# Optimization experiments

Hardware: AMD Instinct MI355X
Metric: run time of the kernel (lower is better)

Reference implementation:

```python
import jax, jax.numpy as jnp
import numpy as np

B, S, H = 16, 512, 2048
NH, NKV = 16, 4
HD = H // NH  # 128


def _rope_tables(seq_len, dim, dtype):
    inv_freq = 1.0 / (10000.0 ** (jnp.arange(0, dim, 2, dtype=jnp.float32) / dim))
    t = jnp.arange(seq_len, dtype=jnp.float32)
    freqs = jnp.einsum('i,j->ij', t, inv_freq)          # [S, HD/2]
    emb = jnp.concatenate([freqs, freqs], axis=-1)       # [S, HD]
    cos = jnp.cos(emb)[None, None].astype(dtype)         # [1,1,S,HD]
    sin = jnp.sin(emb)[None, None].astype(dtype)
    return cos, sin


def _rotate_half(x):
    x1, x2 = jnp.split(x, 2, axis=-1)
    return jnp.concatenate([-x2, x1], axis=-1)


def setup_inputs() -> dict:
    key = jax.random.key(0)
    kx, kq, kk, kv, ko = jax.random.split(key, 5)
    x = jax.random.normal(kx, (B, S, H), dtype=jnp.float32)
    s = 0.02
    Wq = jax.random.normal(kq, (H, H), dtype=jnp.float32) * s
    Wk = jax.random.normal(kk, (NKV * HD, H), dtype=jnp.float32) * s
    Wv = jax.random.normal(kv, (NKV * HD, H), dtype=jnp.float32) * s
    Wo = jax.random.normal(ko, (H, H), dtype=jnp.float32) * s
    return {"x": x, "Wq": Wq, "Wk": Wk, "Wv": Wv, "Wo": Wo}


def reference(x, Wq, Wk, Wv, Wo):
    b, s, _ = x.shape
    scaling = HD ** -0.5
    # projections (torch Linear: y = x @ W.T, W is [out,in])
    q = jnp.einsum('bsh,oh->bso', x, Wq).reshape(b, s, NH, HD).transpose(0, 2, 1, 3)
    k = jnp.einsum('bsh,oh->bso', x, Wk).reshape(b, s, NKV, HD).transpose(0, 2, 1, 3)
    v = jnp.einsum('bsh,oh->bso', x, Wv).reshape(b, s, NKV, HD).transpose(0, 2, 1, 3)
    cos, sin = _rope_tables(s, HD, x.dtype)
    q = q * cos + _rotate_half(q) * sin
    k = k * cos + _rotate_half(k) * sin
    rep = NH // NKV
    k = jnp.repeat(k, rep, axis=1)  # [b, NH, s, HD]
    v = jnp.repeat(v, rep, axis=1)
    scores = jnp.einsum('bhqd,bhkd->bhqk', q, k) * scaling
    attn = jax.nn.softmax(scores, axis=-1)
    out = jnp.einsum('bhqk,bhkd->bhqd', attn, v)
    out = out.transpose(0, 2, 1, 3).reshape(b, s, H)
    return jnp.einsum('bsh,oh->bso', out, Wo)
```

## Files before the change

### kernel.cpp

```cpp
#include <hip/hip_runtime.h>
#include <stdint.h>


typedef _Float16 f16;
typedef _Float16 f16x4 __attribute__((ext_vector_type(4)));
typedef _Float16 f16x8 __attribute__((ext_vector_type(8)));
typedef float f32x4 __attribute__((ext_vector_type(4)));

#define B_   16
#define S_   512
#define H_   2048
#define NH_  16
#define NKV_ 4
#define HD_  128
#define ATT_SCALE 0.08838834764831843f
#define LOG2_10000_DIV64 0.20762050593045952f

#define AS1 __attribute__((address_space(1)))
#define AS3 __attribute__((address_space(3)))

__device__ __forceinline__ void async16(const void* g, const void* l) {
  __builtin_amdgcn_global_load_lds((const AS1 unsigned int*)(uintptr_t)g,
                                   (AS3 unsigned int*)(uintptr_t)l, 16, 0, 0);
}

__global__ __launch_bounds__(256) void cast_all(const float* __restrict__ x,
                                                const float* __restrict__ wq,
                                                const float* __restrict__ wk,
                                                const float* __restrict__ wv,
                                                const float* __restrict__ wo,
                                                f16* __restrict__ x_h,
                                                f16* __restrict__ w_h,
                                                f16* __restrict__ wo_h) {
  const int i = blockIdx.x * 256 + threadIdx.x;
  const float4* src;
  f16x4* dst;
  if (i < 4194304) {
    src = (const float4*)x + i;            dst = (f16x4*)x_h + i;
  } else if (i < 5242880) {
    int j = i - 4194304;
    src = (const float4*)wq + j;           dst = (f16x4*)w_h + j;
  } else if (i < 5505024) {
    int j = i - 5242880;
    src = (const float4*)wk + j;           dst = (f16x4*)w_h + 1048576 + j;
  } else if (i < 5767168) {
    int j = i - 5505024;
    src = (const float4*)wv + j;           dst = (f16x4*)w_h + 1310720 + j;
  } else {
    int j = i - 5767168;
    src = (const float4*)wo + j;           dst = (f16x4*)wo_h + j;
  }
  float4 v = *src;
  f16x4 o = {(f16)v.x, (f16)v.y, (f16)v.z, (f16)v.w};
  *dst = o;
}

__device__ __forceinline__ int swz(int r, int c) { return c ^ ((r >> 1) & 3); }

__global__ __launch_bounds__(256) void gemm_qkv(const f16* __restrict__ A,
                                                const f16* __restrict__ W,
                                                f16* __restrict__ qo,
                                                f16* __restrict__ ko,
                                                f16* __restrict__ vto) {
  __shared__ __align__(16) f16 As[128 * 32];
  __shared__ __align__(16) f16 Bs[128 * 32];
  const int K = 2048;
  const int m0 = blockIdx.x * 128;
  const int n0 = blockIdx.y * 128;
  const int tid = threadIdx.x;
  const int wave = tid >> 6, lane = tid & 63;
  const int quad = lane >> 4, l15 = lane & 15;
  const int wm = wave >> 1, wn = wave & 1;
  const int G0 = wave * 128 + lane;
  const int r0 = G0 >> 2, c0g = swz(r0, G0 & 3);
  const int r1 = (G0 + 64) >> 2, c1g = swz(r1, (G0 + 64) & 3);

  f32x4 acc[4][4] = {};

  for (int k0 = 0; k0 < K; k0 += 32) {
    async16(A + (size_t)(m0 + r0) * K + k0 + c0g * 8, (const char*)As + (size_t)G0 * 16);
    async16(A + (size_t)(m0 + r1) * K + k0 + c1g * 8, (const char*)As + (size_t)(G0 + 64) * 16);
    async16(W + (size_t)(n0 + r0) * K + k0 + c0g * 8, (const char*)Bs + (size_t)G0 * 16);
    async16(W + (size_t)(n0 + r1) * K + k0 + c1g * 8, (const char*)Bs + (size_t)(G0 + 64) * 16);
    __syncthreads();
    f16x8 a[4], b[4];
#pragma unroll
    for (int mi = 0; mi < 4; ++mi) {
      const int row = wm * 64 + mi * 16 + l15;
      a[mi] = *reinterpret_cast<const f16x8*>(As + row * 32 + swz(row, quad) * 8);
    }
#pragma unroll
    for (int ni = 0; ni < 4; ++ni) {
      const int col = (ni >> 1) * 64 + wn * 32 + (ni & 1) * 16 + l15;
      b[ni] = *reinterpret_cast<const f16x8*>(Bs + col * 32 + swz(col, quad) * 8);
    }
#pragma unroll
    for (int mi = 0; mi < 4; ++mi)
#pragma unroll
      for (int ni = 0; ni < 4; ++ni)
        acc[mi][ni] = __builtin_amdgcn_mfma_f32_16x16x32_f16(a[mi], b[ni], acc[mi][ni], 0, 0, 0);
    __syncthreads();
  }

  const int b_ = m0 >> 9;
  if (n0 >= 2560) {
    const int h = (n0 - 2560) >> 7;
    f16* vb = vto + ((size_t)b_ * NKV_ + h) * HD_ * S_;
#pragma unroll
    for (int mi = 0; mi < 4; ++mi)
#pragma unroll
      for (int r = 0; r < 4; ++r) {
        const int s = (m0 + wm * 64 + mi * 16 + quad * 4 + r) & 511;
#pragma unroll
        for (int ni = 0; ni < 4; ++ni) {
          const int d = (ni >> 1) * 64 + wn * 32 + (ni & 1) * 16 + l15;
          vb[(size_t)d * S_ + s] = (f16)acc[mi][ni][r];
        }
      }
  } else {
    f16* ob = (n0 < 2048) ? (qo + ((size_t)b_ * NH_ + (n0 >> 7)) * S_ * HD_)
                          : (ko + ((size_t)b_ * NKV_ + ((n0 - 2048) >> 7)) * S_ * HD_);
    float invf[2];
#pragma unroll
    for (int ni = 0; ni < 2; ++ni)
      invf[ni] = exp2f((float)(wn * 32 + ni * 16 + l15) * -LOG2_10000_DIV64);
#pragma unroll
    for (int mi = 0; mi < 4; ++mi)
#pragma unroll
      for (int r = 0; r < 4; ++r) {
        const int s = (m0 + wm * 64 + mi * 16 + quad * 4 + r) & 511;
        const size_t rb = (size_t)s * HD_;
#pragma unroll
        for (int ni = 0; ni < 2; ++ni) {
          const int d = wn * 32 + ni * 16 + l15;
          float sn, cs;
          __sincosf((float)s * invf[ni], &sn, &cs);
          const float x1 = acc[mi][ni][r], x2 = acc[mi][ni + 2][r];
          ob[rb + d] = (f16)(x1 * cs - x2 * sn);
          ob[rb + d + 64] = (f16)(x2 * cs + x1 * sn);
        }
      }
  }
}

__global__ __launch_bounds__(512) void attn_kernel(const f16* __restrict__ q,
                                                   const f16* __restrict__ k,
                                                   const f16* __restrict__ vt,
                                                   f16* __restrict__ out) {
  __shared__ __align__(16) f16 Qs[128 * 128];
  __shared__ __align__(16) f16 Ks[128 * 128];
  __shared__ __align__(16) f16 Vs[128 * 128];
  __shared__ __align__(16) f16 Ps[8][16 * 136];

  const int qt = blockIdx.x, h = blockIdx.y, b = blockIdx.z;
  const int kvh = h >> 2;
  const int tid = threadIdx.x;
  const int wave = tid >> 6, lane = tid & 63;
  const int quad = lane >> 4, l15 = lane & 15;
  const int sm0 = wave * 16;

  const f16* qbase = q + (((size_t)b * NH_ + h) * S_ + qt * 128) * HD_;
  const f16* kbase = k + ((size_t)b * NKV_ + kvh) * S_ * HD_;
  const f16* vbase = vt + ((size_t)b * NKV_ + kvh) * HD_ * S_;

#pragma unroll
  for (int i = 0; i < 4; ++i) {
    const int L = wave * 256 + i * 64 + lane;
    const int r = L >> 4;
    const int c = (L & 15) ^ (r & 15);
    async16(qbase + (size_t)r * HD_ + c * 8, (const char*)Qs + (size_t)(wave * 256 + i * 64) * 16);
  }

  f32x4 O[8] = {};
  float mrun[4], lrun[4];
#pragma unroll
  for (int r = 0; r < 4; ++r) { mrun[r] = -3.0e38f; lrun[r] = 0.f; }

  for (int j = 0; j < 4; ++j) {
    if (j) __syncthreads();
#pragma unroll
    for (int i = 0; i < 4; ++i) {
      const int L = wave * 256 + i * 64 + lane;
      const int r = L >> 4;
      const int c = (L & 15) ^ (r & 15);
      async16(kbase + (size_t)(j * 128 + r) * HD_ + c * 8,
              (const char*)Ks + (size_t)(wave * 256 + i * 64) * 16);
      async16(vbase + (size_t)r * S_ + j * 128 + c * 8,
              (const char*)Vs + (size_t)(wave * 256 + i * 64) * 16);
    }
    __syncthreads();

    f32x4 Sc[8] = {};
#pragma unroll
    for (int ks = 0; ks < 4; ++ks) {
      f16x8 aq, bk[8];
      aq = *reinterpret_cast<const f16x8*>(Qs + ((sm0 + l15) * 16 + (((ks * 4 + quad) ^ l15))) * 8);
#pragma unroll
      for (int ni = 0; ni < 8; ++ni)
        bk[ni] = *reinterpret_cast<const f16x8*>(Ks + ((ni * 16 + l15) * 16 + ((ks * 4 + quad) ^ l15)) * 8);
#pragma unroll
      for (int ni = 0; ni < 8; ++ni)
        Sc[ni] = __builtin_amdgcn_mfma_f32_16x16x32_f16(aq, bk[ni], Sc[ni], 0, 0, 0);
    }

#pragma unroll
    for (int r = 0; r < 4; ++r) {
      float mx = -3.0e38f;
#pragma unroll
      for (int ni = 0; ni < 8; ++ni) mx = fmaxf(mx, Sc[ni][r]);
      mx *= ATT_SCALE;
#pragma unroll
      for (int off = 1; off < 16; off <<= 1) mx = fmaxf(mx, __shfl_xor(mx, off));
      const float mnew = fmaxf(mrun[r], mx);
      const float alpha = __expf(mrun[r] - mnew);
      float rs = 0.f;
#pragma unroll
      for (int ni = 0; ni < 8; ++ni) {
        const float pv = __expf(Sc[ni][r] * ATT_SCALE - mnew);
        Sc[ni][r] = pv;
        rs += pv;
      }
#pragma unroll
      for (int off = 1; off < 16; off <<= 1) rs += __shfl_xor(rs, off);
      lrun[r] = lrun[r] * alpha + rs;
      mrun[r] = mnew;
#pragma unroll
      for (int ni = 0; ni < 8; ++ni) O[ni][r] *= alpha;
#pragma unroll
      for (int ni = 0; ni < 8; ++ni)
        Ps[wave][(quad * 4 + r) * 136 + ni * 16 + l15] = (f16)Sc[ni][r];
    }

#pragma unroll
    for (int ks = 0; ks < 4; ++ks) {
      f16x8 ap, bv[8];
      ap = *reinterpret_cast<const f16x8*>(&Ps[wave][l15 * 136 + ks * 32 + quad * 8]);
#pragma unroll
      for (int ni = 0; ni < 8; ++ni)
        bv[ni] = *reinterpret_cast<const f16x8*>(Vs + ((ni * 16 + l15) * 16 + ((ks * 4 + quad) ^ l15)) * 8);
#pragma unroll
      for (int ni = 0; ni < 8; ++ni)
        O[ni] = __builtin_amdgcn_mfma_f32_16x16x32_f16(ap, bv[ni], O[ni], 0, 0, 0);
    }
  }

#pragma unroll
  for (int r = 0; r < 4; ++r) {
    const float inv = 1.f / lrun[r];
    const int srow = qt * 128 + sm0 + quad * 4 + r;
#pragma unroll
    for (int ni = 0; ni < 8; ++ni)
      out[((size_t)b * S_ + srow) * H_ + h * HD_ + ni * 16 + l15] = (f16)(O[ni][r] * inv);
  }
}

__global__ __launch_bounds__(256) void gemm_out(const f16* __restrict__ A,
                                                const f16* __restrict__ W,
                                                float* __restrict__ out) {
  __shared__ __align__(16) f16 As[128 * 32];
  __shared__ __align__(16) f16 Bs[128 * 32];
  const int K = 2048;
  const int m0 = blockIdx.x * 128;
  const int n0 = blockIdx.y * 128;
  const int tid = threadIdx.x;
  const int wave = tid >> 6, lane = tid & 63;
  const int quad = lane >> 4, l15 = lane & 15;
  const int wm = wave >> 1, wn = wave & 1;
  const int G0 = wave * 128 + lane;
  const int r0 = G0 >> 2, c0g = swz(r0, G0 & 3);
  const int r1 = (G0 + 64) >> 2, c1g = swz(r1, (G0 + 64) & 3);

  f32x4 acc[4][4] = {};

  for (int k0 = 0; k0 < K; k0 += 32) {
    async16(A + (size_t)(m0 + r0) * K + k0 + c0g * 8, (const char*)As + (size_t)G0 * 16);
    async16(A + (size_t)(m0 + r1) * K + k0 + c1g * 8, (const char*)As + (size_t)(G0 + 64) * 16);
    async16(W + (size_t)(n0 + r0) * K + k0 + c0g * 8, (const char*)Bs + (size_t)G0 * 16);
    async16(W + (size_t)(n0 + r1) * K + k0 + c1g * 8, (const char*)Bs + (size_t)(G0 + 64) * 16);
    __syncthreads();
    f16x8 a[4], b[4];
#pragma unroll
    for (int mi = 0; mi < 4; ++mi) {
      const int row = wm * 64 + mi * 16 + l15;
      a[mi] = *reinterpret_cast<const f16x8*>(As + row * 32 + swz(row, quad) * 8);
    }
#pragma unroll
    for (int ni = 0; ni < 4; ++ni) {
      const int col = wn * 64 + ni * 16 + l15;
      b[ni] = *reinterpret_cast<const f16x8*>(Bs + col * 32 + swz(col, quad) * 8);
    }
#pragma unroll
    for (int mi = 0; mi < 4; ++mi)
#pragma unroll
      for (int ni = 0; ni < 4; ++ni)
        acc[mi][ni] = __builtin_amdgcn_mfma_f32_16x16x32_f16(a[mi], b[ni], acc[mi][ni], 0, 0, 0);
    __syncthreads();
  }

#pragma unroll
  for (int mi = 0; mi < 4; ++mi) {
#pragma unroll
    for (int ni = 0; ni < 4; ++ni) {
      const int ncol = n0 + wn * 64 + ni * 16 + l15;
#pragma unroll
      for (int r = 0; r < 4; ++r) {
        const int mrow = m0 + wm * 64 + mi * 16 + quad * 4 + r;
        out[(size_t)mrow * 2048 + ncol] = acc[mi][ni][r];
      }
    }
  }
}

extern "C" void kernel_launch(void* const* d_in, const int* in_sizes, int n_in,
                              void* d_out, int out_size, void* d_ws, size_t ws_size,
                              hipStream_t stream) {
  const float* x = (const float*)d_in[0];
  const float* Wq = (const float*)d_in[1];
  const float* Wk = (const float*)d_in[2];
  const float* Wv = (const float*)d_in[3];
  const float* Wo = (const float*)d_in[4];
  float* out = (float*)d_out;
  char* ws = (char*)d_ws;

  f16* x_h  = (f16*)(ws + 0);
  f16* w_h  = (f16*)(ws + 33554432);
  f16* wo_h = (f16*)(ws + 46137344);
  f16* qb   = (f16*)(ws + 54525952);
  f16* kb   = (f16*)(ws + 88080384);
  f16* vtb  = (f16*)(ws + 96468992);
  f16* attn = (f16*)(ws + 104857600);

  cast_all<<<26624, 256, 0, stream>>>(x, Wq, Wk, Wv, Wo, x_h, w_h, wo_h);
  gemm_qkv<<<dim3(64, 24), 256, 0, stream>>>(x_h, w_h, qb, kb, vtb);
  attn_kernel<<<dim3(4, 16, 16), 512, 0, stream>>>(qb, kb, vtb, attn);
  gemm_out<<<dim3(64, 16), 256, 0, stream>>>(attn, wo_h, out);
}
```

Measured before the change: 471.0 us.

## Replace both GEMMs with a 256x256-tile, 4-stage async-pipelined templated kernel

Merges the QKV and output projection GEMMs into one templated kernel with 256x256 tiles, 512 threads and a 4-buffer LDS ring of global_load_lds prefetches. The main loop is split into two half-steps, using explicit waitcnt, barriers and setprio so loads overlap with MFMA work. The larger tile is meant to raise operand reuse and hide global-memory latency. In exchange it drops the LDS swizzle, which risks bank conflicts, uses a large accumulator array that may push register pressure, and launches fewer blocks, which may lower CU utilisation (384 and 256 blocks).

```diff
diff --git a/kernel.cpp b/kernel.cpp
--- a/kernel.cpp
+++ b/kernel.cpp
@@ -55,89 +55,149 @@
   *dst = o;
 }
 
-__device__ __forceinline__ int swz(int r, int c) { return c ^ ((r >> 1) & 3); }
-
-__global__ __launch_bounds__(256) void gemm_qkv(const f16* __restrict__ A,
-                                                const f16* __restrict__ W,
-                                                f16* __restrict__ qo,
-                                                f16* __restrict__ ko,
-                                                f16* __restrict__ vto) {
-  __shared__ __align__(16) f16 As[128 * 32];
-  __shared__ __align__(16) f16 Bs[128 * 32];
+template<int MODE>
+__global__ __launch_bounds__(512, 2) void gemm256(const f16* __restrict__ A,
+                                                  const f16* __restrict__ W,
+                                                  f16* __restrict__ qo,
+                                                  f16* __restrict__ ko,
+                                                  f16* __restrict__ vto,
+                                                  float* __restrict__ fout) {
+  __shared__ __align__(16) f16 As[4][256 * 32];
+  __shared__ __align__(16) f16 Bs[4][256 * 32];
   const int K = 2048;
-  const int m0 = blockIdx.x * 128;
-  const int n0 = blockIdx.y * 128;
+  const int NT = 64;
+  const int m0 = blockIdx.x * 256;
+  const int n0 = blockIdx.y * 256;
   const int tid = threadIdx.x;
   const int wave = tid >> 6, lane = tid & 63;
   const int quad = lane >> 4, l15 = lane & 15;
-  const int wm = wave >> 1, wn = wave & 1;
-  const int G0 = wave * 128 + lane;
-  const int r0 = G0 >> 2, c0g = swz(r0, G0 & 3);
-  const int r1 = (G0 + 64) >> 2, c1g = swz(r1, (G0 + 64) & 3);
-
-  f32x4 acc[4][4] = {};
-
-  for (int k0 = 0; k0 < K; k0 += 32) {
-    async16(A + (size_t)(m0 + r0) * K + k0 + c0g * 8, (const char*)As + (size_t)G0 * 16);
-    async16(A + (size_t)(m0 + r1) * K + k0 + c1g * 8, (const char*)As + (size_t)(G0 + 64) * 16);
-    async16(W + (size_t)(n0 + r0) * K + k0 + c0g * 8, (const char*)Bs + (size_t)G0 * 16);
-    async16(W + (size_t)(n0 + r1) * K + k0 + c1g * 8, (const char*)Bs + (size_t)(G0 + 64) * 16);
-    __syncthreads();
-    f16x8 a[4], b[4];
-#pragma unroll
-    for (int mi = 0; mi < 4; ++mi) {
-      const int row = wm * 64 + mi * 16 + l15;
-      a[mi] = *reinterpret_cast<const f16x8*>(As + row * 32 + swz(row, quad) * 8);
-    }
+  const int wm = wave >> 2, wn = wave & 3;
+
+  const f16* aptr = A + (size_t)(m0 + (tid >> 2)) * K + (tid & 3) * 8;
+  const f16* bptr = W + (size_t)(n0 + (tid >> 2)) * K + (tid & 3) * 8;
+  const int ldst = wave * 1024;
+
+  f32x4 acc[8][4] = {};
+
+#pragma unroll
+  for (int t = 0; t < 3; ++t) {
+    const int k0 = t * 32;
+    async16(aptr + k0,             (const char*)&As[t][0] + ldst);
+    async16(aptr + 128 * K + k0,   (const char*)&As[t][0] + 8192 + ldst);
+    async16(bptr + k0,             (const char*)&Bs[t][0] + ldst);
+    async16(bptr + 128 * K + k0,   (const char*)&Bs[t][0] + 8192 + ldst);
+  }
+  asm volatile("s_waitcnt vmcnt(8)" ::: "memory");
+  __builtin_amdgcn_s_barrier();
+
+  for (int t = 0; t < NT; ++t) {
+    const int buf = t & 3;
+    const f16* Ab = &As[buf][0];
+    const f16* Bb = &Bs[buf][0];
+    const int sbuf = (t + 3) & 3;
+    const int sk0 = (t + 3) * 32;
+    f16x8 afr[4], bfr[4];
+
+#pragma unroll
+    for (int mi = 0; mi < 4; ++mi)
+      afr[mi] = *reinterpret_cast<const f16x8*>(Ab + (wm * 128 + mi * 16 + l15) * 32 + quad * 8);
 #pragma unroll
     for (int ni = 0; ni < 4; ++ni) {
-      const int col = (ni >> 1) * 64 + wn * 32 + (ni & 1) * 16 + l15;
-      b[ni] = *reinterpret_cast<const f16x8*>(Bs + col * 32 + swz(col, quad) * 8);
-    }
+      const int col = MODE ? ((wn >> 1) * 128 + (ni >> 1) * 64 + (wn & 1) * 32 + (ni & 1) * 16 + l15)
+                           : (wn * 64 + ni * 16 + l15);
+      bfr[ni] = *reinterpret_cast<const f16x8*>(Bb + col * 32 + quad * 8);
+    }
+    if (t + 3 < NT) {
+      async16(aptr + sk0,           (const char*)&As[sbuf][0] + ldst);
+      async16(aptr + 128 * K + sk0, (const char*)&As[sbuf][0] + 8192 + ldst);
+    }
+    __builtin_amdgcn_s_barrier();
+    asm volatile("s_waitcnt lgkmcnt(0)" ::: "memory");
+    __builtin_amdgcn_sched_barrier(0);
+    __builtin_amdgcn_s_setprio(1);
 #pragma unroll
     for (int mi = 0; mi < 4; ++mi)
 #pragma unroll
       for (int ni = 0; ni < 4; ++ni)
-        acc[mi][ni] = __builtin_amdgcn_mfma_f32_16x16x32_f16(a[mi], b[ni], acc[mi][ni], 0, 0, 0);
-    __syncthreads();
-  }
-
-  const int b_ = m0 >> 9;
-  if (n0 >= 2560) {
-    const int h = (n0 - 2560) >> 7;
-    f16* vb = vto + ((size_t)b_ * NKV_ + h) * HD_ * S_;
+        acc[mi][ni] = __builtin_amdgcn_mfma_f32_16x16x32_f16(afr[mi], bfr[ni], acc[mi][ni], 0, 0, 0);
+    __builtin_amdgcn_s_setprio(0);
+    __builtin_amdgcn_s_barrier();
+
 #pragma unroll
     for (int mi = 0; mi < 4; ++mi)
-#pragma unroll
-      for (int r = 0; r < 4; ++r) {
-        const int s = (m0 + wm * 64 + mi * 16 + quad * 4 + r) & 511;
-#pragma unroll
-        for (int ni = 0; ni < 4; ++ni) {
-          const int d = (ni >> 1) * 64 + wn * 32 + (ni & 1) * 16 + l15;
-          vb[(size_t)d * S_ + s] = (f16)acc[mi][ni][r];
+      afr[mi] = *reinterpret_cast<const f16x8*>(Ab + (wm * 128 + (mi + 4) * 16 + l15) * 32 + quad * 8);
+    if (t + 3 < NT) {
+      async16(bptr + sk0,           (const char*)&Bs[sbuf][0] + ldst);
+      async16(bptr + 128 * K + sk0, (const char*)&Bs[sbuf][0] + 8192 + ldst);
+    }
+    __builtin_amdgcn_s_barrier();
+    asm volatile("s_waitcnt lgkmcnt(0)" ::: "memory");
+    __builtin_amdgcn_sched_barrier(0);
+    __builtin_amdgcn_s_setprio(1);
+#pragma unroll
+    for (int mi = 0; mi < 4; ++mi)
+#pragma unroll
+      for (int ni = 0; ni < 4; ++ni)
+        acc[mi + 4][ni] = __builtin_amdgcn_mfma_f32_16x16x32_f16(afr[mi], bfr[ni], acc[mi + 4][ni], 0, 0, 0);
+    __builtin_amdgcn_s_setprio(0);
+
+    if (t + 3 < NT)      asm volatile("s_waitcnt vmcnt(8)" ::: "memory");
+    else if (t + 2 < NT) asm volatile("s_waitcnt vmcnt(4)" ::: "memory");
+    else if (t + 1 < NT) asm volatile("s_waitcnt vmcnt(0)" ::: "memory");
+    __builtin_amdgcn_s_barrier();
+  }
+
+  if constexpr (MODE == 1) {
+    const int b_ = m0 >> 9;
+    if (n0 >= 2560) {
+      const int h = ((n0 - 2560) >> 7) + (wn >> 1);
+      f16* vb = vto + ((size_t)b_ * NKV_ + h) * HD_ * S_;
+#pragma unroll
+      for (int mi = 0; mi < 8; ++mi)
+#pragma unroll
+        for (int r = 0; r < 4; ++r) {
+          const int s = (m0 + wm * 128 + mi * 16 + quad * 4 + r) & 511;
+#pragma unroll
+          for (int ni = 0; ni < 4; ++ni) {
+            const int d = (ni >> 1) * 64 + (wn & 1) * 32 + (ni & 1) * 16 + l15;
+            vb[(size_t)d * S_ + s] = (f16)acc[mi][ni][r];
+          }
         }
-      }
+    } else {
+      f16* ob = (n0 < 2048)
+          ? (qo + ((size_t)b_ * NH_ + (n0 >> 7) + (wn >> 1)) * S_ * HD_)
+          : (ko + ((size_t)b_ * NKV_ + ((n0 - 2048) >> 7) + (wn >> 1)) * S_ * HD_);
+      float invf[2];
+#pragma unroll
+      for (int ni = 0; ni < 2; ++ni)
+        invf[ni] = exp2f((float)((wn & 1) * 32 + ni * 16 + l15) * -LOG2_10000_DIV64);
+#pragma unroll
+      for (int mi = 0; mi < 8; ++mi)
+#pragma unroll
+        for (int r = 0; r < 4; ++r) {
+          const int s = (m0 + wm * 128 + mi * 16 + quad * 4 + r) & 511;
+          const size_t rb = (size_t)s * HD_;
+#pragma unroll
+          for (int ni = 0; ni < 2; ++ni) {
+            const int d = (wn & 1) * 32 + ni * 16 + l15;
+            float sn, cs;
+            __sincosf((float)s * invf[ni], &sn, &cs);
+            const float x1 = acc[mi][ni][r], x2 = acc[mi][ni + 2][r];
+            ob[rb + d] = (f16)(x1 * cs - x2 * sn);
+            ob[rb + d + 64] = (f16)(x2 * cs + x1 * sn);
+          }
+        }
+    }
   } else {
-    f16* ob = (n0 < 2048) ? (qo + ((size_t)b_ * NH_ + (n0 >> 7)) * S_ * HD_)
-                          : (ko + ((size_t)b_ * NKV_ + ((n0 - 2048) >> 7)) * S_ * HD_);
-    float invf[2];
-#pragma unroll
-    for (int ni = 0; ni < 2; ++ni)
-      invf[ni] = exp2f((float)(wn * 32 + ni * 16 + l15) * -LOG2_10000_DIV64);
-#pragma unroll
-    for (int mi = 0; mi < 4; ++mi)
-#pragma unroll
-      for (int r = 0; r < 4; ++r) {
-        const int s = (m0 + wm * 64 + mi * 16 + quad * 4 + r) & 511;
-        const size_t rb = (size_t)s * HD_;
-#pragma unroll
-        for (int ni = 0; ni < 2; ++ni) {
-          const int d = wn * 32 + ni * 16 + l15;
-          float sn, cs;
-          __sincosf((float)s * invf[ni], &sn, &cs);
-          const float x1 = acc[mi][ni][r], x2 = acc[mi][ni + 2][r];
-          ob[rb + d] = (f16)(x1 * cs - x2 * sn);
-          ob[rb + d + 64] = (f16)(x2 * cs + x1 * sn);
+#pragma unroll
+    for (int mi = 0; mi < 8; ++mi)
+#pragma unroll
+      for (int ni = 0; ni < 4; ++ni) {
+        const int ncol = n0 + wn * 64 + ni * 16 + l15;
+#pragma unroll
+        for (int r = 0; r < 4; ++r) {
+          const int mrow = m0 + wm * 128 + mi * 16 + quad * 4 + r;
+          fout[(size_t)mrow * 2048 + ncol] = acc[mi][ni][r];
         }
       }
   }
@@ -251,63 +311,6 @@
 #pragma unroll
     for (int ni = 0; ni < 8; ++ni)
       out[((size_t)b * S_ + srow) * H_ + h * HD_ + ni * 16 + l15] = (f16)(O[ni][r] * inv);
-  }
-}
-
-__global__ __launch_bounds__(256) void gemm_out(const f16* __restrict__ A,
-                                                const f16* __restrict__ W,
-                                                float* __restrict__ out) {
-  __shared__ __align__(16) f16 As[128 * 32];
-  __shared__ __align__(16) f16 Bs[128 * 32];
-  const int K = 2048;
-  const int m0 = blockIdx.x * 128;
-  const int n0 = blockIdx.y * 128;
-  const int tid = threadIdx.x;
-  const int wave = tid >> 6, lane = tid & 63;
-  const int quad = lane >> 4, l15 = lane & 15;
-  const int wm = wave >> 1, wn = wave & 1;
-  const int G0 = wave * 128 + lane;
-  const int r0 = G0 >> 2, c0g = swz(r0, G0 & 3);
-  const int r1 = (G0 + 64) >> 2, c1g = swz(r1, (G0 + 64) & 3);
-
-  f32x4 acc[4][4] = {};
-
-  for (int k0 = 0; k0 < K; k0 += 32) {
-    async16(A + (size_t)(m0 + r0) * K + k0 + c0g * 8, (const char*)As + (size_t)G0 * 16);
-    async16(A + (size_t)(m0 + r1) * K + k0 + c1g * 8, (const char*)As + (size_t)(G0 + 64) * 16);
-    async16(W + (size_t)(n0 + r0) * K + k0 + c0g * 8, (const char*)Bs + (size_t)G0 * 16);
-    async16(W + (size_t)(n0 + r1) * K + k0 + c1g * 8, (const char*)Bs + (size_t)(G0 + 64) * 16);
-    __syncthreads();
-    f16x8 a[4], b[4];
-#pragma unroll
-    for (int mi = 0; mi < 4; ++mi) {
-      const int row = wm * 64 + mi * 16 + l15;
-      a[mi] = *reinterpret_cast<const f16x8*>(As + row * 32 + swz(row, quad) * 8);
-    }
-#pragma unroll
-    for (int ni = 0; ni < 4; ++ni) {
-      const int col = wn * 64 + ni * 16 + l15;
-      b[ni] = *reinterpret_cast<const f16x8*>(Bs + col * 32 + swz(col, quad) * 8);
-    }
-#pragma unroll
-    for (int mi = 0; mi < 4; ++mi)
-#pragma unroll
-      for (int ni = 0; ni < 4; ++ni)
-        acc[mi][ni] = __builtin_amdgcn_mfma_f32_16x16x32_f16(a[mi], b[ni], acc[mi][ni], 0, 0, 0);
-    __syncthreads();
-  }
-
-#pragma unroll
-  for (int mi = 0; mi < 4; ++mi) {
-#pragma unroll
-    for (int ni = 0; ni < 4; ++ni) {
-      const int ncol = n0 + wn * 64 + ni * 16 + l15;
-#pragma unroll
-      for (int r = 0; r < 4; ++r) {
-        const int mrow = m0 + wm * 64 + mi * 16 + quad * 4 + r;
-        out[(size_t)mrow * 2048 + ncol] = acc[mi][ni][r];
-      }
-    }
   }
 }
 
@@ -331,7 +334,7 @@
   f16* attn = (f16*)(ws + 104857600);
 
   cast_all<<<26624, 256, 0, stream>>>(x, Wq, Wk, Wv, Wo, x_h, w_h, wo_h);
-  gemm_qkv<<<dim3(64, 24), 256, 0, stream>>>(x_h, w_h, qb, kb, vtb);
+  gemm256<1><<<dim3(32, 12), 512, 0, stream>>>(x_h, w_h, qb, kb, vtb, nullptr);
   attn_kernel<<<dim3(4, 16, 16), 512, 0, stream>>>(qb, kb, vtb, attn);
-  gemm_out<<<dim3(64, 16), 256, 0, stream>>>(attn, wo_h, out);
-}
+  gemm256<0><<<dim3(32, 8), 512, 0, stream>>>(attn, wo_h, nullptr, nullptr, nullptr, out);
+}
```

Measured after the change: 427.2 us. 9.3% less time.
